# Kernel tuning notes

Hardware: AMD Instinct MI355X
Metric: run time of the kernel (lower is better)

## Reference

```python
import jax, jax.numpy as jnp
import numpy as np

EPS = 1e-5
N_NODES = 100000
N_EDGES = 1000000
N_MAP = 128
N_SCALES = 2
N_BLK = 2


def group_norm(x, g, b):
    # GroupNorm(ng=1) on [N, C]: normalize over channel dim per row
    mu = jnp.mean(x, axis=-1, keepdims=True)
    var = jnp.mean(jnp.square(x - mu), axis=-1, keepdims=True)
    return (x - mu) * jax.lax.rsqrt(var + EPS) * g + b


def lin_gn(x, w, g, b, act=True):
    h = group_norm(x @ w, g, b)
    return jax.nn.relu(h) if act else h


def linear_res(x, w1, g1, b1, w2, g2, b2, wt, gt, bt):
    out = lin_gn(x, w1, g1, b1, act=True)
    out = group_norm(out @ w2, g2, b2)
    out = out + group_norm(x @ wt, gt, bt)  # transform path (22 != 128)
    return jax.nn.relu(out)


def scatter_max0(src, idx, n):
    # torch_scatter.scatter_max with dim_size=n: empty segments -> 0
    m = jax.ops.segment_max(src, idx, num_segments=n)
    return jnp.where(jnp.isneginf(m), 0.0, m)


def agg_block(agt, u, v, w1, g1, b1, w2, g2, b2, wl, gl, bl):
    res = agt
    ctx = lin_gn(agt, w1, g1, b1, act=True)[u]          # [E, C] gather
    agg = scatter_max0(ctx, v, agt.shape[0])            # [N, C] scatter_max
    h = lin_gn(jnp.concatenate([agt, agg], axis=1), w2, g2, b2, act=True)
    h = lin_gn(h, wl, gl, bl, act=False)
    return jax.nn.relu(h + res)


def setup_inputs() -> dict:
    key = jax.random.key(0)
    ks = jax.random.split(key, 24)
    d = {}
    d['feats'] = jax.random.normal(ks[0], (N_NODES, 22), dtype=jnp.float32)
    d['u'] = jax.random.randint(ks[1], (N_SCALES, N_EDGES), 0, N_NODES)
    d['v'] = jax.random.randint(ks[2], (N_SCALES, N_EDGES), 0, N_NODES)
    def w(k, shape, scale):
        return jax.random.normal(k, shape, dtype=jnp.float32) * scale
    d['in_w1'] = w(ks[3], (22, N_MAP), 22 ** -0.5)
    d['in_g1'] = jax.random.uniform(ks[4], (N_MAP,), minval=0.5, maxval=1.5)
    d['in_b1'] = w(ks[5], (N_MAP,), 0.02)
    d['in_w2'] = w(ks[6], (N_MAP, N_MAP), N_MAP ** -0.5)
    d['in_g2'] = jax.random.uniform(ks[7], (N_MAP,), minval=0.5, maxval=1.5)
    d['in_b2'] = w(ks[8], (N_MAP,), 0.02)
    d['in_wt'] = w(ks[9], (22, N_MAP), 22 ** -0.5)
    d['in_gt'] = jax.random.uniform(ks[10], (N_MAP,), minval=0.5, maxval=1.5)
    d['in_bt'] = w(ks[11], (N_MAP,), 0.02)
    nb = N_BLK * N_SCALES
    d['fc1_w'] = w(ks[12], (nb, N_MAP, N_MAP), N_MAP ** -0.5)
    d['fc1_g'] = jax.random.uniform(ks[13], (nb, N_MAP), minval=0.5, maxval=1.5)
    d['fc1_b'] = w(ks[14], (nb, N_MAP), 0.02)
    d['fc2_w'] = w(ks[15], (nb, 2 * N_MAP, N_MAP), (2 * N_MAP) ** -0.5)
    d['fc2_g'] = jax.random.uniform(ks[16], (nb, N_MAP), minval=0.5, maxval=1.5)
    d['fc2_b'] = w(ks[17], (nb, N_MAP), 0.02)
    d['lin_w'] = w(ks[18], (nb, N_MAP, N_MAP), N_MAP ** -0.5)
    d['lin_g'] = jax.random.uniform(ks[19], (nb, N_MAP), minval=0.5, maxval=1.5)
    d['lin_b'] = w(ks[20], (nb, N_MAP), 0.02)
    return d


def reference(feats, u, v, in_w1, in_g1, in_b1, in_w2, in_g2, in_b2,
              in_wt, in_gt, in_bt, fc1_w, fc1_g, fc1_b, fc2_w, fc2_g, fc2_b,
              lin_w, lin_g, lin_b):
    feat = linear_res(feats, in_w1, in_g1, in_b1, in_w2, in_g2, in_b2,
                      in_wt, in_gt, in_bt)
    for j in range(N_BLK):
        for i in range(N_SCALES):
            k = j * N_SCALES + i
            feat = agg_block(feat, u[i], v[i],
                             fc1_w[k], fc1_g[k], fc1_b[k],
                             fc2_w[k], fc2_g[k], fc2_b[k],
                             lin_w[k], lin_g[k], lin_b[k])
    return feat
```

## Files before the change

### kernel.cpp

```cpp
#include <hip/hip_runtime.h>

#define NMAP 128
#define EPSV 1e-5f
#define SCHUNK 2048
#define HSTR 136
#define BKSH 8
#define CH 8192

typedef __attribute__((ext_vector_type(8))) short bf16x8;
typedef __attribute__((ext_vector_type(4))) float f32x4;

__device__ __forceinline__ unsigned short f2bf(float f) {
    union { float f; unsigned u; } x; x.f = f;
    unsigned u = x.u;
    return (unsigned short)((u + 0x7fffu + ((u >> 16) & 1u)) >> 16);
}
__device__ __forceinline__ float bf2f(unsigned short h) {
    union { unsigned u; float f; } x; x.u = ((unsigned)h) << 16;
    return x.f;
}
__device__ __forceinline__ unsigned cvt_pk_bf16(float lo, float hi) {
    unsigned r;
    asm("v_cvt_pk_bf16_f32 %0, %1, %2" : "=v"(r) : "v"(lo), "v"(hi));
    return r;
}
__device__ __forceinline__ unsigned pkmax(unsigned a, unsigned b) {
    unsigned r;
    asm("v_pk_max_u16 %0, %1, %2" : "=v"(r) : "v"(a), "v"(b));
    return r;
}
__device__ __forceinline__ uint4 pkmax4(uint4 a, uint4 b) {
    return make_uint4(pkmax(a.x, b.x), pkmax(a.y, b.y),
                      pkmax(a.z, b.z), pkmax(a.w, b.w));
}

struct __align__(16) FSmem {
    unsigned short h[32 * HSTR];
    unsigned short res[32 * HSTR];
    float2 red[4][4][34];
    float mv[32][2];
};

__device__ __forceinline__ void gn_stats(FSmem& s, const f32x4 acc[2][2],
                                         int w, int l15, int lhi, int tid)
{
    const int cg = l15 >> 2;
    #pragma unroll
    for (int mi = 0; mi < 2; ++mi) {
        #pragma unroll
        for (int j = 0; j < 4; ++j) {
            float a0 = acc[mi][0][j], a1 = acc[mi][1][j];
            float s0 = a0 + a1, s1 = a0 * a0 + a1 * a1;
            s0 += __shfl_xor(s0, 1); s1 += __shfl_xor(s1, 1);
            s0 += __shfl_xor(s0, 2); s1 += __shfl_xor(s1, 2);
            if ((l15 & 3) == 0) {
                int row = mi * 16 + lhi * 4 + j;
                s.red[w][cg][row] = make_float2(s0, s1);
            }
        }
    }
    __syncthreads();
    if (tid < 32) {
        float sm = 0.f, ss = 0.f;
        #pragma unroll
        for (int ww = 0; ww < 4; ++ww)
            #pragma unroll
            for (int cgg = 0; cgg < 4; ++cgg) {
                float2 p = s.red[ww][cgg][tid];
                sm += p.x; ss += p.y;
            }
        float mean = sm * (1.f / 128.f);
        float var = ss * (1.f / 128.f) - mean * mean;
        s.mv[tid][0] = mean;
        s.mv[tid][1] = rsqrtf(var + EPSV);
    }
    __syncthreads();
}

__device__ __forceinline__ void gemm_lds(f32x4 acc[2][2], const FSmem& s,
    const unsigned short* __restrict__ WT, int K, int kwoff, int nks,
    int w, int l15, int lhi)
{
    #pragma unroll
    for (int ks = 0; ks < nks; ++ks) {
        bf16x8 af[2], bfr[2];
        #pragma unroll
        for (int mi = 0; mi < 2; ++mi)
            af[mi] = *(const bf16x8*)&s.h[(mi * 16 + l15) * HSTR + ks * 32 + lhi * 8];
        #pragma unroll
        for (int ni = 0; ni < 2; ++ni)
            bfr[ni] = *(const bf16x8*)&WT[(size_t)(w * 32 + ni * 16 + l15) * K + kwoff + ks * 32 + lhi * 8];
        #pragma unroll
        for (int mi = 0; mi < 2; ++mi)
            #pragma unroll
            for (int ni = 0; ni < 2; ++ni)
                acc[mi][ni] = __builtin_amdgcn_mfma_f32_16x16x32_bf16(
                    af[mi], bfr[ni], acc[mi][ni], 0, 0, 0);
    }
}

__device__ __forceinline__ void gemm_feat_stash(f32x4 acc[2][2], FSmem& s,
    const unsigned short* __restrict__ Xf,
    const unsigned short* __restrict__ WT,
    int rowbase, int w, int l15, int lhi)
{
    #pragma unroll
    for (int ks = 0; ks < 4; ++ks) {
        bf16x8 af[2], bfr[2];
        #pragma unroll
        for (int mi = 0; mi < 2; ++mi)
            af[mi] = *(const bf16x8*)&Xf[(size_t)(rowbase + mi * 16 + l15) * 128 + ks * 32 + lhi * 8];
        if (w == 0) {
            #pragma unroll
            for (int mi = 0; mi < 2; ++mi)
                *(bf16x8*)&s.res[(mi * 16 + l15) * HSTR + ks * 32 + lhi * 8] = af[mi];
        }
        #pragma unroll
        for (int ni = 0; ni < 2; ++ni)
            bfr[ni] = *(const bf16x8*)&WT[(size_t)(w * 32 + ni * 16 + l15) * 256 + ks * 32 + lhi * 8];
        #pragma unroll
        for (int mi = 0; mi < 2; ++mi)
            #pragma unroll
            for (int ni = 0; ni < 2; ++ni)
                acc[mi][ni] = __builtin_amdgcn_mfma_f32_16x16x32_bf16(
                    af[mi], bfr[ni], acc[mi][ni], 0, 0, 0);
    }
}

__device__ __forceinline__ void epi_lds(const f32x4 acc[2][2], FSmem& s,
    const float* __restrict__ g, const float* __restrict__ b, int w, int l15, int lhi)
{
    float gv[2], bv[2];
    #pragma unroll
    for (int ni = 0; ni < 2; ++ni) {
        int col = w * 32 + ni * 16 + l15;
        gv[ni] = g[col]; bv[ni] = b[col];
    }
    #pragma unroll
    for (int mi = 0; mi < 2; ++mi)
        #pragma unroll
        for (int j = 0; j < 4; ++j) {
            int row = mi * 16 + lhi * 4 + j;
            float mean = s.mv[row][0], rstd = s.mv[row][1];
            float v0 = fmaxf((acc[mi][0][j] - mean) * rstd * gv[0] + bv[0], 0.f);
            float v1 = fmaxf((acc[mi][1][j] - mean) * rstd * gv[1] + bv[1], 0.f);
            unsigned pk = cvt_pk_bf16(v0, v1);
            int c0 = w * 32 + l15;
            s.h[row * HSTR + c0]      = (unsigned short)pk;
            s.h[row * HSTR + c0 + 16] = (unsigned short)(pk >> 16);
        }
}

__device__ __forceinline__ void norm_reg(f32x4 acc[2][2], const FSmem& s,
    const float* __restrict__ g, const float* __restrict__ b, int w, int l15, int lhi)
{
    float gv[2], bv[2];
    #pragma unroll
    for (int ni = 0; ni < 2; ++ni) {
        int col = w * 32 + ni * 16 + l15;
        gv[ni] = g[col]; bv[ni] = b[col];
    }
    #pragma unroll
    for (int mi = 0; mi < 2; ++mi)
        #pragma unroll
        for (int j = 0; j < 4; ++j) {
            int row = mi * 16 + lhi * 4 + j;
            float mean = s.mv[row][0], rstd = s.mv[row][1];
            #pragma unroll
            for (int ni = 0; ni < 2; ++ni)
                acc[mi][ni][j] = (acc[mi][ni][j] - mean) * rstd * gv[ni] + bv[ni];
        }
}

__device__ __forceinline__ void vec_out(const unsigned short* __restrict__ t,
    unsigned short* __restrict__ dst, int rowbase, int nrows, int tid)
{
    #pragma unroll
    for (int it = 0; it < 2; ++it) {
        int c = tid * 2 + it;
        int row = c >> 4, col8 = (c & 15) * 8;
        if (rowbase + row < nrows)
            *(bf16x8*)&dst[(size_t)(rowbase + row) * NMAP + col8] =
                *(const bf16x8*)&t[row * HSTR + col8];
    }
}

__global__ __launch_bounds__(256) void input_fused(
    const unsigned short* __restrict__ X32,
    const unsigned short* __restrict__ wts,
    const float* __restrict__ g1, const float* __restrict__ b1,
    const float* __restrict__ gt, const float* __restrict__ bt,
    const float* __restrict__ g2, const float* __restrict__ b2,
    const float* __restrict__ g1n, const float* __restrict__ b1n,
    unsigned short* __restrict__ fbf, unsigned short* __restrict__ h1bf,
    int nrows)
{
    __shared__ FSmem s;
    const int tid = threadIdx.x;
    const int w = tid >> 6, l = tid & 63, l15 = l & 15, lhi = l >> 4;
    const int rowbase = blockIdx.x * 32;

    const unsigned short* w1T = wts;
    const unsigned short* wtT = wts + 4096;
    const unsigned short* w2T = wts + 8192;
    const unsigned short* f1T = wts + 24576;

    f32x4 accA[2][2] = {}, accT[2][2] = {};
    {
        bf16x8 af[2], b1f[2], btf[2];
        #pragma unroll
        for (int mi = 0; mi < 2; ++mi)
            af[mi] = *(const bf16x8*)&X32[(size_t)(rowbase + mi * 16 + l15) * 32 + lhi * 8];
        #pragma unroll
        for (int ni = 0; ni < 2; ++ni) {
            int col = w * 32 + ni * 16 + l15;
            b1f[ni] = *(const bf16x8*)&w1T[(size_t)col * 32 + lhi * 8];
            btf[ni] = *(const bf16x8*)&wtT[(size_t)col * 32 + lhi * 8];
        }
        #pragma unroll
        for (int mi = 0; mi < 2; ++mi)
            #pragma unroll
            for (int ni = 0; ni < 2; ++ni) {
                accA[mi][ni] = __builtin_amdgcn_mfma_f32_16x16x32_bf16(af[mi], b1f[ni], accA[mi][ni], 0, 0, 0);
                accT[mi][ni] = __builtin_amdgcn_mfma_f32_16x16x32_bf16(af[mi], btf[ni], accT[mi][ni], 0, 0, 0);
            }
    }

    gn_stats(s, accT, w, l15, lhi, tid);
    norm_reg(accT, s, gt, bt, w, l15, lhi);
    gn_stats(s, accA, w, l15, lhi, tid);
    epi_lds(accA, s, g1, b1, w, l15, lhi);
    __syncthreads();

    f32x4 accB[2][2] = {};
    gemm_lds(accB, s, w2T, 128, 0, 4, w, l15, lhi);
    gn_stats(s, accB, w, l15, lhi, tid);
    {
        float gv[2], bv[2];
        #pragma unroll
        for (int ni = 0; ni < 2; ++ni) {
            int col = w * 32 + ni * 16 + l15;
            gv[ni] = g2[col]; bv[ni] = b2[col];
        }
        #pragma unroll
        for (int mi = 0; mi < 2; ++mi)
            #pragma unroll
            for (int j = 0; j < 4; ++j) {
                int rl = mi * 16 + lhi * 4 + j;
                float mean = s.mv[rl][0], rstd = s.mv[rl][1];
                float v0 = fmaxf((accB[mi][0][j] - mean) * rstd * gv[0] + bv[0]
                                 + accT[mi][0][j], 0.f);
                float v1 = fmaxf((accB[mi][1][j] - mean) * rstd * gv[1] + bv[1]
                                 + accT[mi][1][j], 0.f);
                unsigned pk = cvt_pk_bf16(v0, v1);
                int c0 = w * 32 + l15;
                s.h[rl * HSTR + c0]      = (unsigned short)pk;
                s.h[rl * HSTR + c0 + 16] = (unsigned short)(pk >> 16);
            }
    }
    __syncthreads();

    f32x4 accC[2][2] = {};
    gemm_lds(accC, s, f1T, 128, 0, 4, w, l15, lhi);
    gn_stats(s, accC, w, l15, lhi, tid);
    vec_out(s.h, fbf, rowbase, nrows, tid);
    {
        float gv[2], bv[2];
        #pragma unroll
        for (int ni = 0; ni < 2; ++ni) {
            int col = w * 32 + ni * 16 + l15;
            gv[ni] = g1n[col]; bv[ni] = b1n[col];
        }
        #pragma unroll
        for (int mi = 0; mi < 2; ++mi)
            #pragma unroll
            for (int j = 0; j < 4; ++j) {
                int rl = mi * 16 + lhi * 4 + j;
                float mean = s.mv[rl][0], rstd = s.mv[rl][1];
                float v0 = fmaxf((accC[mi][0][j] - mean) * rstd * gv[0] + bv[0], 0.f);
                float v1 = fmaxf((accC[mi][1][j] - mean) * rstd * gv[1] + bv[1], 0.f);
                unsigned pk = cvt_pk_bf16(v0, v1);
                int c0 = w * 32 + l15;
                s.res[rl * HSTR + c0]      = (unsigned short)pk;
                s.res[rl * HSTR + c0 + 16] = (unsigned short)(pk >> 16);
            }
    }
    __syncthreads();
    vec_out(s.res, h1bf, rowbase, nrows, tid);
}

__global__ __launch_bounds__(256) void block_fused(
    unsigned short* __restrict__ fbf,
    const int* __restrict__ rp, const int* __restrict__ su,
    const unsigned* __restrict__ h1in,
    const unsigned short* __restrict__ wts, int kblk,
    const float* __restrict__ g2, const float* __restrict__ b2,
    const float* __restrict__ gl, const float* __restrict__ bl,
    const float* __restrict__ g1n, const float* __restrict__ b1n,
    unsigned short* __restrict__ h1out, float* __restrict__ outf,
    int nrows, int has_next)
{
    __shared__ FSmem s;
    const int tid = threadIdx.x;
    const int w = tid >> 6, l = tid & 63, l15 = l & 15, lhi = l >> 4;
    const int rowbase = blockIdx.x * 32;

    const unsigned short* fc2T = wts + 90112 + (size_t)kblk * 32768;
    const unsigned short* linT = wts + 221184 + (size_t)kblk * 16384;
    const unsigned short* f1T  = wts + 24576 + (size_t)(kblk + 1) * 16384;

    {
        const int node8 = tid >> 3, g = tid & 7;
        const int node = rowbase + node8;
        uint4 A0 = make_uint4(0, 0, 0, 0), A1 = make_uint4(0, 0, 0, 0);
        uint4 B0 = make_uint4(0, 0, 0, 0), B1 = make_uint4(0, 0, 0, 0);
        if (node < nrows) {
            int j = rp[node], e0 = rp[node + 1];
            for (; j + 3 < e0; j += 4) {
                const uint4* r0 = (const uint4*)&h1in[(size_t)su[j] * 64 + g * 8];
                const uint4* r1 = (const uint4*)&h1in[(size_t)su[j + 1] * 64 + g * 8];
                const uint4* r2 = (const uint4*)&h1in[(size_t)su[j + 2] * 64 + g * 8];
                const uint4* r3 = (const uint4*)&h1in[(size_t)su[j + 3] * 64 + g * 8];
                uint4 x0 = r0[0], x1 = r0[1];
                uint4 y0 = r1[0], y1 = r1[1];
                uint4 z0 = r2[0], z1 = r2[1];
                uint4 q0 = r3[0], q1 = r3[1];
                A0 = pkmax4(A0, x0); A1 = pkmax4(A1, x1);
                B0 = pkmax4(B0, y0); B1 = pkmax4(B1, y1);
                A0 = pkmax4(A0, z0); A1 = pkmax4(A1, z1);
                B0 = pkmax4(B0, q0); B1 = pkmax4(B1, q1);
            }
            for (; j < e0; ++j) {
                const uint4* r0 = (const uint4*)&h1in[(size_t)su[j] * 64 + g * 8];
                A0 = pkmax4(A0, r0[0]); A1 = pkmax4(A1, r0[1]);
            }
            A0 = pkmax4(A0, B0); A1 = pkmax4(A1, B1);
        }
        *(uint4*)&s.h[node8 * HSTR + g * 16]     = A0;
        *(uint4*)&s.h[node8 * HSTR + g * 16 + 8] = A1;
    }
    __syncthreads();

    f32x4 acc2[2][2] = {};
    gemm_feat_stash(acc2, s, fbf, fc2T, rowbase, w, l15, lhi);
    gemm_lds(acc2, s, fc2T, 256, 128, 4, w, l15, lhi);
    gn_stats(s, acc2, w, l15, lhi, tid);
    epi_lds(acc2, s, g2, b2, w, l15, lhi);
    __syncthreads();

    f32x4 acc3[2][2] = {};
    gemm_lds(acc3, s, linT, 128, 0, 4, w, l15, lhi);
    gn_stats(s, acc3, w, l15, lhi, tid);
    {
        float gv[2], bv[2];
        #pragma unroll
        for (int ni = 0; ni < 2; ++ni) {
            int col = w * 32 + ni * 16 + l15;
            gv[ni] = gl[col]; bv[ni] = bl[col];
        }
        #pragma unroll
        for (int mi = 0; mi < 2; ++mi)
            #pragma unroll
            for (int j = 0; j < 4; ++j) {
                int rl = mi * 16 + lhi * 4 + j;
                int row = rowbase + rl;
                float mean = s.mv[rl][0], rstd = s.mv[rl][1];
                int c0 = w * 32 + l15;
                float v0 = (acc3[mi][0][j] - mean) * rstd * gv[0] + bv[0]
                         + bf2f(s.res[rl * HSTR + c0]);
                float v1 = (acc3[mi][1][j] - mean) * rstd * gv[1] + bv[1]
                         + bf2f(s.res[rl * HSTR + c0 + 16]);
                v0 = fmaxf(v0, 0.f); v1 = fmaxf(v1, 0.f);
                unsigned pk = cvt_pk_bf16(v0, v1);
                s.h[rl * HSTR + c0]      = (unsigned short)pk;
                s.h[rl * HSTR + c0 + 16] = (unsigned short)(pk >> 16);
                if (outf && row < nrows) {
                    outf[(size_t)row * NMAP + c0]      = v0;
                    outf[(size_t)row * NMAP + c0 + 16] = v1;
                }
            }
    }

    if (has_next) {
        __syncthreads();
        f32x4 acc4[2][2] = {};
        gemm_lds(acc4, s, f1T, 128, 0, 4, w, l15, lhi);
        gn_stats(s, acc4, w, l15, lhi, tid);
        vec_out(s.h, fbf, rowbase, nrows, tid);
        {
            float gv[2], bv[2];
            #pragma unroll
            for (int ni = 0; ni < 2; ++ni) {
                int col = w * 32 + ni * 16 + l15;
                gv[ni] = g1n[col]; bv[ni] = b1n[col];
            }
            #pragma unroll
            for (int mi = 0; mi < 2; ++mi)
                #pragma unroll
                for (int j = 0; j < 4; ++j) {
                    int rl = mi * 16 + lhi * 4 + j;
                    float mean = s.mv[rl][0], rstd = s.mv[rl][1];
                    float v0 = fmaxf((acc4[mi][0][j] - mean) * rstd * gv[0] + bv[0], 0.f);
                    float v1 = fmaxf((acc4[mi][1][j] - mean) * rstd * gv[1] + bv[1], 0.f);
                    unsigned pk = cvt_pk_bf16(v0, v1);
                    int c0 = w * 32 + l15;
                    s.res[rl * HSTR + c0]      = (unsigned short)pk;
                    s.res[rl * HSTR + c0 + 16] = (unsigned short)(pk >> 16);
                }
        }
        __syncthreads();
        vec_out(s.res, h1out, rowbase, nrows, tid);
    }
}

__global__ __launch_bounds__(256) void cvt_all_w(
    const float* __restrict__ in_w1, const float* __restrict__ in_wt,
    const float* __restrict__ in_w2, const float* __restrict__ fc1_w,
    const float* __restrict__ fc2_w, const float* __restrict__ lin_w,
    unsigned short* __restrict__ wts)
{
    int idx = blockIdx.x * 256 + threadIdx.x;
    if (idx >= 286720) return;
    const float* src; int off, K, Kreal;
    if (idx < 4096)        { src = in_w1; off = idx;          K = 32;  Kreal = 22; }
    else if (idx < 8192)   { src = in_wt; off = idx - 4096;   K = 32;  Kreal = 22; }
    else if (idx < 24576)  { src = in_w2; off = idx - 8192;   K = 128; Kreal = 128; }
    else if (idx < 90112)  { src = fc1_w; off = idx - 24576;  K = 128; Kreal = 128; }
    else if (idx < 221184) { src = fc2_w; off = idx - 90112;  K = 256; Kreal = 256; }
    else                   { src = lin_w; off = idx - 221184; K = 128; Kreal = 128; }
    int per = 128 * K;
    int m = off / per, rem = off - m * per;
    int c = rem / K, k = rem - c * K;
    float val = (k < Kreal) ? src[(size_t)m * per + (size_t)k * 128 + c] : 0.f;
    wts[idx] = f2bf(val);
}

__global__ __launch_bounds__(256) void cvt_feats_kernel(
    const float* __restrict__ src, unsigned short* __restrict__ dst, int N)
{
    int idx = blockIdx.x * 256 + threadIdx.x;
    int n = idx >> 5, kk = idx & 31;
    if (n < N + 64) {
        float v = (n < N && kk < 22) ? src[(size_t)n * 22 + kk] : 0.f;
        dst[idx] = f2bf(v);
    }
}

__global__ __launch_bounds__(256) void hist2_kernel(
    const int* __restrict__ v, int* __restrict__ rp, int E, int N)
{
    int e = blockIdx.x * 256 + threadIdx.x;
    if (e < 2 * E) {
        int sc = e >= E;
        atomicAdd(&rp[sc * (N + 1) + v[e] + 1], 1);
    }
}

__global__ __launch_bounds__(256) void scan1_kernel(
    int* __restrict__ rp, int* __restrict__ part, int n1, int NB)
{
    __shared__ int wtot[4];
    const int sc = blockIdx.x / NB, chunk = blockIdx.x - sc * NB;
    int* data = rp + (size_t)sc * n1;
    const int tid = threadIdx.x;
    const int base = chunk * SCHUNK + tid * 8;
    int vv[8];
    #pragma unroll
    for (int i = 0; i < 8; ++i) {
        int idx = base + i;
        vv[i] = (idx < n1) ? data[idx] : 0;
    }
    #pragma unroll
    for (int i = 1; i < 8; ++i) vv[i] += vv[i - 1];
    int tsum = vv[7];
    const int lane = tid & 63, wid = tid >> 6;
    int scn = tsum;
    #pragma unroll
    for (int d = 1; d < 64; d <<= 1) {
        int t = __shfl_up(scn, d);
        if (lane >= d) scn += t;
    }
    if (lane == 63) wtot[wid] = scn;
    __syncthreads();
    int woff = 0;
    for (int w2 = 0; w2 < wid; ++w2) woff += wtot[w2];
    const int excl = scn - tsum + woff;
    #pragma unroll
    for (int i = 0; i < 8; ++i) {
        int idx = base + i;
        if (idx < n1) data[idx] = vv[i] + excl;
    }
    if (tid == 255) part[blockIdx.x] = excl + tsum;
}

__global__ __launch_bounds__(256) void scan2_kernel(int* part, int NB)
{
    __shared__ int wsum[4];
    int* data = part + blockIdx.x * NB;
    const int tid = threadIdx.x;
    const int lane = tid & 63, wid = tid >> 6;
    int carry = 0;
    for (int base = 0; base < NB; base += 256) {
        int i = base + tid;
        int val = (i < NB) ? data[i] : 0;
        #pragma unroll
        for (int d = 1; d < 64; d <<= 1) {
            int t = __shfl_up(val, d);
            if (lane >= d) val += t;
        }
        if (lane == 63) wsum[wid] = val;
        __syncthreads();
        int woff = 0;
        for (int w = 0; w < wid; ++w) woff += wsum[w];
        int total = wsum[0] + wsum[1] + wsum[2] + wsum[3];
        val += woff + carry;
        if (i < NB) data[i] = val;
        __syncthreads();
        carry += total;
    }
}

__global__ __launch_bounds__(256) void scan3_kernel(
    int* __restrict__ rp, const int* __restrict__ part, int n1, int NB)
{
    const int nbm1 = NB - 1;
    const int sc = blockIdx.x / nbm1, i = blockIdx.x - sc * nbm1;
    int* data = rp + (size_t)sc * n1;
    const int base = (i + 1) * SCHUNK + threadIdx.x * 8;
    const int off = part[sc * NB + i];
    #pragma unroll
    for (int q = 0; q < 8; ++q) {
        int idx = base + q;
        if (idx < n1) data[idx] += off;
    }
}

__global__ __launch_bounds__(256) void init_gcur(
    const int* __restrict__ rp, int* __restrict__ gcur, int E, int N, int nbk)
{
    int i = blockIdx.x * 256 + threadIdx.x;
    if (i < 2 * nbk) {
        int sc = i >= nbk;
        int b = i - sc * nbk;
        int nb0 = b << BKSH; if (nb0 > N) nb0 = N;
        gcur[i] = sc * E + rp[sc * (N + 1) + nb0];
    }
}

__global__ __launch_bounds__(256) void bucket_scatter(
    const int* __restrict__ u, const int* __restrict__ v,
    int* __restrict__ gcur, unsigned* __restrict__ pairs, int E, int nbk)
{
    __shared__ int cnt[1024], base[1024];
    const int tid = threadIdx.x;
    const int tot = 2 * E;
    const int c0 = blockIdx.x * CH;
    const int nbk2 = 2 * nbk;
    for (int i = tid; i < nbk2; i += 256) cnt[i] = 0;
    __syncthreads();
    for (int i = 0; i < CH; i += 256) {
        int e = c0 + i + tid;
        if (e < tot) {
            int sc = e >= E;
            int vv = v[e];
            atomicAdd(&cnt[sc * nbk + (vv >> BKSH)], 1);
        }
    }
    __syncthreads();
    for (int i = tid; i < nbk2; i += 256) {
        int c = cnt[i];
        base[i] = c ? atomicAdd(&gcur[i], c) : 0;
        cnt[i] = 0;
    }
    __syncthreads();
    for (int i = 0; i < CH; i += 256) {
        int e = c0 + i + tid;
        if (e < tot) {
            int sc = e >= E;
            unsigned uu = (unsigned)u[e];
            int vv = v[e];
            int bk = sc * nbk + (vv >> BKSH);
            int off = atomicAdd(&cnt[bk], 1);
            pairs[(size_t)base[bk] + off] =
                uu | ((unsigned)(vv & ((1 << BKSH) - 1)) << 24);
        }
    }
}

__global__ __launch_bounds__(256) void bucket_fill(
    const unsigned* __restrict__ pairs, const int* __restrict__ rp,
    int* __restrict__ su, int E, int N, int nbk)
{
    __shared__ int curs[256];
    const int bk = blockIdx.x;
    const int sc = bk >= nbk;
    const int b = bk - sc * nbk;
    const int nb0 = b << BKSH;
    const int nb1 = min(nb0 + (1 << BKSH), N);
    const int nn = nb1 - nb0;
    const int* rps = rp + (size_t)sc * (N + 1);
    const int tid = threadIdx.x;
    const int rstart = rps[nb0], rend = rps[nb1];
    if (tid < nn) curs[tid] = rps[nb0 + tid];
    __syncthreads();
    int* sus = su + (size_t)sc * E;
    for (int idx = rstart + tid; idx < rend; idx += 256) {
        unsigned pr = pairs[(size_t)sc * E + idx];
        int vloc = (int)(pr >> 24);
        int pos = atomicAdd(&curs[vloc], 1);
        sus[pos] = (int)(pr & 0x00FFFFFFu);
    }
}

extern "C" void kernel_launch(void* const* d_in, const int* in_sizes, int n_in,
                              void* d_out, int out_size, void* d_ws, size_t ws_size,
                              hipStream_t stream)
{
    const float* feats = (const float*)d_in[0];
    const int*   u     = (const int*)d_in[1];
    const int*   v     = (const int*)d_in[2];
    const float* in_w1 = (const float*)d_in[3];
    const float* in_g1 = (const float*)d_in[4];
    const float* in_b1 = (const float*)d_in[5];
    const float* in_w2 = (const float*)d_in[6];
    const float* in_g2 = (const float*)d_in[7];
    const float* in_b2 = (const float*)d_in[8];
    const float* in_wt = (const float*)d_in[9];
    const float* in_gt = (const float*)d_in[10];
    const float* in_bt = (const float*)d_in[11];
    const float* fc1_w = (const float*)d_in[12];
    const float* fc1_g = (const float*)d_in[13];
    const float* fc1_b = (const float*)d_in[14];
    const float* fc2_w = (const float*)d_in[15];
    const float* fc2_g = (const float*)d_in[16];
    const float* fc2_b = (const float*)d_in[17];
    const float* lin_w = (const float*)d_in[18];
    const float* lin_g = (const float*)d_in[19];
    const float* lin_b = (const float*)d_in[20];

    const int N = in_sizes[0] / 22;
    const int E = in_sizes[1] / 2;
    const size_t nmp = (size_t)(N + 64) * NMAP;

    unsigned short* fbf  = (unsigned short*)d_ws;
    unsigned short* h1A  = fbf + nmp;
    unsigned short* h1B  = h1A + nmp;
    unsigned short* x32  = h1B + nmp;
    unsigned short* wts  = x32 + (size_t)(N + 64) * 32;
    unsigned short* wend = wts + 286720;

    int* rp   = (int*)wend;
    int* su   = rp + 2 * (N + 1);
    int* part = su + 2 * (size_t)E;
    int* gcur = part + 256;
    unsigned* pairs = (unsigned*)h1B;

    const int nbk = (N + (1 << BKSH) - 1) >> BKSH;

    cvt_feats_kernel<<<((N + 64) * 32 + 255) / 256, 256, 0, stream>>>(feats, x32, N);
    cvt_all_w<<<(286720 + 255) / 256, 256, 0, stream>>>(
        in_w1, in_wt, in_w2, fc1_w, fc2_w, lin_w, wts);

    {
        const int n1 = N + 1;
        const int NB = (n1 + SCHUNK - 1) / SCHUNK;
        hipMemsetAsync(rp, 0, 2 * (size_t)n1 * sizeof(int), stream);
        hist2_kernel<<<(2 * E + 255) / 256, 256, 0, stream>>>(v, rp, E, N);
        scan1_kernel<<<2 * NB, 256, 0, stream>>>(rp, part, n1, NB);
        scan2_kernel<<<2, 256, 0, stream>>>(part, NB);
        scan3_kernel<<<2 * (NB - 1), 256, 0, stream>>>(rp, part, n1, NB);
        init_gcur<<<(2 * nbk + 255) / 256, 256, 0, stream>>>(rp, gcur, E, N, nbk);
        bucket_scatter<<<(2 * E + CH - 1) / CH, 256, 0, stream>>>(
            u, v, gcur, pairs, E, nbk);
        bucket_fill<<<2 * nbk, 256, 0, stream>>>(pairs, rp, su, E, N, nbk);
    }

    const int GB = (N + 31) / 32;

    input_fused<<<GB, 256, 0, stream>>>(x32, wts,
        in_g1, in_b1, in_gt, in_bt, in_g2, in_b2,
        fc1_g, fc1_b, fbf, h1A, N);

    for (int k = 0; k < 4; ++k) {
        int is = k & 1;
        int has_next = (k < 3);
        unsigned short* h1in  = (k & 1) ? h1B : h1A;
        unsigned short* h1out = (k & 1) ? h1A : h1B;
        block_fused<<<GB, 256, 0, stream>>>(fbf,
            rp + (size_t)is * (N + 1), su + (size_t)is * E,
            (const unsigned*)h1in, wts, k,
            fc2_g + k * 128, fc2_b + k * 128,
            lin_g + k * 128, lin_b + k * 128,
            has_next ? fc1_g + (k + 1) * 128 : nullptr,
            has_next ? fc1_b + (k + 1) * 128 : nullptr,
            h1out, (k == 3) ? (float*)d_out : nullptr, N, has_next);
    }
}
```

Measured before the change: 602.2 us.

## Replace per-node histogram and three-pass scan with bucket-level counting

The CSR build no longer runs a global per-node atomic histogram followed by a three-kernel prefix scan. It now counts edges per 256-node bucket with shared-memory atomics and scans the roughly 800 bucket counts in a single block. Each bucket block then recomputes its per-node counts locally, scans them, and writes both row pointers and sorted sources. This drops several launches and the global atomics on 2M edges, at the cost of reading the pairs twice inside bucket_fill2.

```diff
diff --git a/kernel.cpp b/kernel.cpp
--- a/kernel.cpp
+++ b/kernel.cpp
@@ -2,7 +2,6 @@
 
 #define NMAP 128
 #define EPSV 1e-5f
-#define SCHUNK 2048
 #define HSTR 136
 #define BKSH 8
 #define CH 8192
@@ -446,104 +445,55 @@
     }
 }
 
-__global__ __launch_bounds__(256) void hist2_kernel(
-    const int* __restrict__ v, int* __restrict__ rp, int E, int N)
-{
-    int e = blockIdx.x * 256 + threadIdx.x;
-    if (e < 2 * E) {
-        int sc = e >= E;
-        atomicAdd(&rp[sc * (N + 1) + v[e] + 1], 1);
-    }
-}
-
-__global__ __launch_bounds__(256) void scan1_kernel(
-    int* __restrict__ rp, int* __restrict__ part, int n1, int NB)
-{
-    __shared__ int wtot[4];
-    const int sc = blockIdx.x / NB, chunk = blockIdx.x - sc * NB;
-    int* data = rp + (size_t)sc * n1;
+
+__global__ __launch_bounds__(256) void bucket_cnt(
+    const int* __restrict__ v, int* __restrict__ gcnt, int E, int nbk)
+{
+    __shared__ int cnt[1024];
     const int tid = threadIdx.x;
-    const int base = chunk * SCHUNK + tid * 8;
-    int vv[8];
-    #pragma unroll
-    for (int i = 0; i < 8; ++i) {
-        int idx = base + i;
-        vv[i] = (idx < n1) ? data[idx] : 0;
-    }
-    #pragma unroll
-    for (int i = 1; i < 8; ++i) vv[i] += vv[i - 1];
-    int tsum = vv[7];
-    const int lane = tid & 63, wid = tid >> 6;
-    int scn = tsum;
-    #pragma unroll
-    for (int d = 1; d < 64; d <<= 1) {
-        int t = __shfl_up(scn, d);
-        if (lane >= d) scn += t;
-    }
-    if (lane == 63) wtot[wid] = scn;
-    __syncthreads();
-    int woff = 0;
-    for (int w2 = 0; w2 < wid; ++w2) woff += wtot[w2];
-    const int excl = scn - tsum + woff;
-    #pragma unroll
-    for (int i = 0; i < 8; ++i) {
-        int idx = base + i;
-        if (idx < n1) data[idx] = vv[i] + excl;
-    }
-    if (tid == 255) part[blockIdx.x] = excl + tsum;
-}
-
-__global__ __launch_bounds__(256) void scan2_kernel(int* part, int NB)
+    const int tot = 2 * E;
+    const int c0 = blockIdx.x * CH;
+    const int nbk2 = 2 * nbk;
+    for (int i = tid; i < nbk2; i += 256) cnt[i] = 0;
+    __syncthreads();
+    for (int i = 0; i < CH; i += 256) {
+        int e = c0 + i + tid;
+        if (e < tot) {
+            int sc = e >= E;
+            atomicAdd(&cnt[sc * nbk + (v[e] >> BKSH)], 1);
+        }
+    }
+    __syncthreads();
+    for (int i = tid; i < nbk2; i += 256)
+        if (cnt[i]) atomicAdd(&gcnt[i], cnt[i]);
+}
+
+__global__ __launch_bounds__(256) void scan_buckets(
+    const int* __restrict__ gcnt, int* __restrict__ gbase,
+    int* __restrict__ gcur, int n)
 {
     __shared__ int wsum[4];
-    int* data = part + blockIdx.x * NB;
     const int tid = threadIdx.x;
     const int lane = tid & 63, wid = tid >> 6;
     int carry = 0;
-    for (int base = 0; base < NB; base += 256) {
+    for (int base = 0; base < n; base += 256) {
         int i = base + tid;
-        int val = (i < NB) ? data[i] : 0;
+        int val = (i < n) ? gcnt[i] : 0;
+        int inc = val;
         #pragma unroll
         for (int d = 1; d < 64; d <<= 1) {
-            int t = __shfl_up(val, d);
-            if (lane >= d) val += t;
-        }
-        if (lane == 63) wsum[wid] = val;
+            int t = __shfl_up(inc, d);
+            if (lane >= d) inc += t;
+        }
+        if (lane == 63) wsum[wid] = inc;
         __syncthreads();
         int woff = 0;
         for (int w = 0; w < wid; ++w) woff += wsum[w];
         int total = wsum[0] + wsum[1] + wsum[2] + wsum[3];
-        val += woff + carry;
-        if (i < NB) data[i] = val;
+        int excl = inc - val + woff + carry;
+        if (i < n) { gbase[i] = excl; gcur[i] = excl; }
         __syncthreads();
         carry += total;
-    }
-}
-
-__global__ __launch_bounds__(256) void scan3_kernel(
-    int* __restrict__ rp, const int* __restrict__ part, int n1, int NB)
-{
-    const int nbm1 = NB - 1;
-    const int sc = blockIdx.x / nbm1, i = blockIdx.x - sc * nbm1;
-    int* data = rp + (size_t)sc * n1;
-    const int base = (i + 1) * SCHUNK + threadIdx.x * 8;
-    const int off = part[sc * NB + i];
-    #pragma unroll
-    for (int q = 0; q < 8; ++q) {
-        int idx = base + q;
-        if (idx < n1) data[idx] += off;
-    }
-}
-
-__global__ __launch_bounds__(256) void init_gcur(
-    const int* __restrict__ rp, int* __restrict__ gcur, int E, int N, int nbk)
-{
-    int i = blockIdx.x * 256 + threadIdx.x;
-    if (i < 2 * nbk) {
-        int sc = i >= nbk;
-        int b = i - sc * nbk;
-        int nb0 = b << BKSH; if (nb0 > N) nb0 = N;
-        gcur[i] = sc * E + rp[sc * (N + 1) + nb0];
     }
 }
 
@@ -587,27 +537,51 @@
     }
 }
 
-__global__ __launch_bounds__(256) void bucket_fill(
-    const unsigned* __restrict__ pairs, const int* __restrict__ rp,
-    int* __restrict__ su, int E, int N, int nbk)
-{
-    __shared__ int curs[256];
+__global__ __launch_bounds__(256) void bucket_fill2(
+    const unsigned* __restrict__ pairs, const int* __restrict__ gbase,
+    const int* __restrict__ gcnt, int* __restrict__ su, int* __restrict__ rp,
+    int E, int N, int nbk)
+{
+    __shared__ int ncnt[256];
+    __shared__ int wtot[4];
     const int bk = blockIdx.x;
     const int sc = bk >= nbk;
     const int b = bk - sc * nbk;
     const int nb0 = b << BKSH;
     const int nb1 = min(nb0 + (1 << BKSH), N);
     const int nn = nb1 - nb0;
-    const int* rps = rp + (size_t)sc * (N + 1);
     const int tid = threadIdx.x;
-    const int rstart = rps[nb0], rend = rps[nb1];
-    if (tid < nn) curs[tid] = rps[nb0 + tid];
+    const int start = gbase[bk];
+    const int cntb = gcnt[bk];
+    const int lbase = start - sc * E;
+    ncnt[tid] = 0;
+    __syncthreads();
+    for (int idx = start + tid; idx < start + cntb; idx += 256)
+        atomicAdd(&ncnt[pairs[idx] >> 24], 1);
+    __syncthreads();
+    int val = ncnt[tid];
+    int inc = val;
+    const int lane = tid & 63, wid = tid >> 6;
+    #pragma unroll
+    for (int d = 1; d < 64; d <<= 1) {
+        int t = __shfl_up(inc, d);
+        if (lane >= d) inc += t;
+    }
+    if (lane == 63) wtot[wid] = inc;
+    __syncthreads();
+    int woff = 0;
+    for (int w2 = 0; w2 < wid; ++w2) woff += wtot[w2];
+    int excl = inc - val + woff;
+    int* rps = rp + (size_t)sc * (N + 1);
+    if (tid < nn) rps[nb0 + tid] = lbase + excl;
+    if (b == nbk - 1 && tid == 0) rps[N] = E;
+    __syncthreads();
+    ncnt[tid] = lbase + excl;
     __syncthreads();
     int* sus = su + (size_t)sc * E;
-    for (int idx = rstart + tid; idx < rend; idx += 256) {
-        unsigned pr = pairs[(size_t)sc * E + idx];
-        int vloc = (int)(pr >> 24);
-        int pos = atomicAdd(&curs[vloc], 1);
+    for (int idx = start + tid; idx < start + cntb; idx += 256) {
+        unsigned pr = pairs[idx];
+        int pos = atomicAdd(&ncnt[pr >> 24], 1);
         sus[pos] = (int)(pr & 0x00FFFFFFu);
     }
 }
@@ -649,10 +623,11 @@
     unsigned short* wts  = x32 + (size_t)(N + 64) * 32;
     unsigned short* wend = wts + 286720;
 
-    int* rp   = (int*)wend;
-    int* su   = rp + 2 * (N + 1);
-    int* part = su + 2 * (size_t)E;
-    int* gcur = part + 256;
+    int* rp    = (int*)wend;
+    int* su    = rp + 2 * (N + 1);
+    int* gcnt  = su + 2 * (size_t)E;
+    int* gbase = gcnt + 1024;
+    int* gcur  = gbase + 1024;
     unsigned* pairs = (unsigned*)h1B;
 
     const int nbk = (N + (1 << BKSH) - 1) >> BKSH;
@@ -662,17 +637,12 @@
         in_w1, in_wt, in_w2, fc1_w, fc2_w, lin_w, wts);
 
     {
-        const int n1 = N + 1;
-        const int NB = (n1 + SCHUNK - 1) / SCHUNK;
-        hipMemsetAsync(rp, 0, 2 * (size_t)n1 * sizeof(int), stream);
-        hist2_kernel<<<(2 * E + 255) / 256, 256, 0, stream>>>(v, rp, E, N);
-        scan1_kernel<<<2 * NB, 256, 0, stream>>>(rp, part, n1, NB);
-        scan2_kernel<<<2, 256, 0, stream>>>(part, NB);
-        scan3_kernel<<<2 * (NB - 1), 256, 0, stream>>>(rp, part, n1, NB);
-        init_gcur<<<(2 * nbk + 255) / 256, 256, 0, stream>>>(rp, gcur, E, N, nbk);
+        hipMemsetAsync(gcnt, 0, 2 * (size_t)nbk * sizeof(int), stream);
+        bucket_cnt<<<(2 * E + CH - 1) / CH, 256, 0, stream>>>(v, gcnt, E, nbk);
+        scan_buckets<<<1, 256, 0, stream>>>(gcnt, gbase, gcur, 2 * nbk);
         bucket_scatter<<<(2 * E + CH - 1) / CH, 256, 0, stream>>>(
             u, v, gcur, pairs, E, nbk);
-        bucket_fill<<<2 * nbk, 256, 0, stream>>>(pairs, rp, su, E, N, nbk);
+        bucket_fill2<<<2 * nbk, 256, 0, stream>>>(pairs, gbase, gcnt, su, rp, E, N, nbk);
     }
 
     const int GB = (N + 31) / 32;
```

After: 524.2 us. -13.0%, faster.
